# Kernel optimization log

Measured on AMD Instinct MI355X. Metric: run time of the kernel, lower is better.

## Reference

```python
import jax, jax.numpy as jnp
import numpy as np

N = 262144   # total packed tokens
B = 4096     # number of ragged segments
D = 256      # relation_embed_dim
A = 128      # attention_dim


def setup_inputs() -> dict:
    key = jax.random.key(0)
    k1, k2, k3 = jax.random.split(key, 3)
    relation_embeds = jax.random.normal(k1, (N, D), dtype=jnp.float32)
    # ragged segment ends: B-1 random interior end positions + final position N-1
    rng = np.random.default_rng(0)
    ends = np.sort(rng.choice(N - 1, size=B - 1, replace=False))
    ends = np.concatenate([ends, [N - 1]])
    queries_np = np.zeros((N,), dtype=np.int32)
    queries_np[ends] = 1
    queries = jnp.asarray(queries_np)
    # torch nn.Linear weights: [out, in]
    Wq = jax.random.normal(k2, (A, D), dtype=jnp.float32) / np.sqrt(D)
    Wk = jax.random.normal(k3, (A, D), dtype=jnp.float32) / np.sqrt(D)
    return {"relation_embeds": relation_embeds, "queries": queries,
            "num_segments": B, "Wq": Wq, "Wk": Wk}


def reference(relation_embeds, queries, num_segments, Wq, Wk):
    # segment id per token: exclusive cumsum of end markers
    q = queries.astype(jnp.int32)
    seg = jnp.cumsum(q) - q                      # [N] in [0, num_segments)
    ends = jnp.flatnonzero(q, size=num_segments) # [B] last index of each segment
    # per-segment query = Q(last row of segment); per-token key = K(row)
    q_end = relation_embeds[ends] @ Wq.T         # [B, A]
    k = relation_embeds @ Wk.T                   # [N, A]
    logits = jnp.sum(k * q_end[seg], axis=-1)    # [N] dot(Q_seg, K_token)
    # softmax over each ragged segment (dim=0 within segment)
    m = jax.ops.segment_max(logits, seg, num_segments=num_segments)
    ex = jnp.exp(logits - m[seg])
    denom = jax.ops.segment_sum(ex, seg, num_segments=num_segments)
    return ex / denom[seg]                       # [N] concatenated scores
```

## Files before the change

kernel.cpp:

```cpp
#include <hip/hip_runtime.h>
#include <math.h>
#include <float.h>

constexpr int N = 262144;
constexpr int B = 4096;
constexpr int D = 256;
constexpr int A = 128;

constexpr int CHUNK  = 1024;
constexpr int NCHUNK = N / CHUNK;
constexpr int SEGB   = 8;

typedef float fvec4 __attribute__((ext_vector_type(4)));

__global__ void k_partials_M(const int* __restrict__ q, int* __restrict__ partials,
                             const float* __restrict__ Wq, const float* __restrict__ Wk,
                             float* __restrict__ M) {
    int t = threadIdx.x;
    if (blockIdx.x < NCHUNK) {
        int4 v = ((const int4*)q)[blockIdx.x * (CHUNK / 4) + t];
        int s = v.x + v.y + v.z + v.w;
        int lane = t & 63, w = t >> 6;
#pragma unroll
        for (int o = 32; o > 0; o >>= 1) s += __shfl_xor(s, o, 64);
        __shared__ int ws_[4];
        if (lane == 0) ws_[w] = s;
        __syncthreads();
        if (t == 0) partials[blockIdx.x] = ws_[0] + ws_[1] + ws_[2] + ws_[3];
    } else {
        int d1 = blockIdx.x - NCHUNK;
        int d2 = t;
        float acc = 0.f;
#pragma unroll 4
        for (int a = 0; a < A; a++) {
            acc = fmaf(Wk[a * D + d1], Wq[a * D + d2], acc);
        }
        M[d1 * D + d2] = acc;
    }
}

__global__ void k_seg_ends(const int* __restrict__ q, const int* __restrict__ partials,
                           int* __restrict__ seg, int* __restrict__ ends) {
    int t = threadIdx.x;
    int lane = t & 63, w = t >> 6;
    int bid = blockIdx.x;
    int p = partials[t];
    int4 v = ((const int4*)q)[bid * (CHUNK / 4) + t];
    int tsum = v.x + v.y + v.z + v.w;
    int ps = p, ts = tsum;
#pragma unroll
    for (int o = 1; o < 64; o <<= 1) {
        int po = __shfl_up(ps, o, 64);
        int to = __shfl_up(ts, o, 64);
        if (lane >= o) { ps += po; ts += to; }
    }
    __shared__ int wp[4], wt[4];
    __shared__ int offs_sm;
    if (lane == 63) { wp[w] = ps; wt[w] = ts; }
    __syncthreads();
    int addp = 0, addt = 0;
#pragma unroll
    for (int i = 0; i < 4; i++) {
        if (i < w) { addp += wp[i]; addt += wt[i]; }
    }
    int sp_incl = ps + addp;
    int sm_incl = ts + addt;
    if (bid > 0 && t == bid - 1) offs_sm = sp_incl;
    if (bid == 0 && t == 0) offs_sm = 0;
    __syncthreads();
    int run = offs_sm + sm_incl - tsum;
    int base_idx = bid * CHUNK + t * 4;
    int qq[4] = {v.x, v.y, v.z, v.w};
#pragma unroll
    for (int k = 0; k < 4; k++) {
        int idx = base_idx + k;
        seg[idx] = run;
        if (qq[k]) { ends[run] = idx; run++; }
    }
}

__global__ void k_compute_V(const float* __restrict__ X, const int* __restrict__ ends,
                            const float* __restrict__ M, float* __restrict__ V) {
    int t = threadIdx.x;
    int b0 = blockIdx.x * SEGB;
    const float4* xr[SEGB];
#pragma unroll
    for (int r = 0; r < SEGB; r++) {
        xr[r] = (const float4*)(X + (size_t)ends[b0 + r] * D);
    }
    const float4* Mrow = (const float4*)(M + t * D);
    float acc[SEGB];
#pragma unroll
    for (int r = 0; r < SEGB; r++) acc[r] = 0.f;
#pragma unroll 4
    for (int j = 0; j < D / 4; j++) {
        float4 m4 = Mrow[j];
#pragma unroll
        for (int r = 0; r < SEGB; r++) {
            float4 x4 = xr[r][j];
            acc[r] = fmaf(m4.x, x4.x, fmaf(m4.y, x4.y,
                     fmaf(m4.z, x4.z, fmaf(m4.w, x4.w, acc[r]))));
        }
    }
#pragma unroll
    for (int r = 0; r < SEGB; r++) V[(size_t)(b0 + r) * D + t] = acc[r];
}

__global__ void k_logits(const float* __restrict__ X, const int* __restrict__ seg,
                         const float* __restrict__ V, float* __restrict__ logits) {
    int wave = threadIdx.x >> 6;
    int lane = threadIdx.x & 63;
    int tok0 = (blockIdx.x * 4 + wave) * 2;
    const fvec4* xa_p = (const fvec4*)(X + (size_t)tok0 * D) + lane;
    const fvec4* xb_p = (const fvec4*)(X + (size_t)(tok0 + 1) * D) + lane;
    fvec4 xa = __builtin_nontemporal_load(xa_p);
    fvec4 xb = __builtin_nontemporal_load(xb_p);
    int sa = seg[tok0];
    int sb = seg[tok0 + 1];
    float4 va = ((const float4*)(V + (size_t)sa * D))[lane];
    float4 vb = ((const float4*)(V + (size_t)sb * D))[lane];
    float pa = fmaf(xa.x, va.x, fmaf(xa.y, va.y, fmaf(xa.z, va.z, xa.w * va.w)));
    float pb = fmaf(xb.x, vb.x, fmaf(xb.y, vb.y, fmaf(xb.z, vb.z, xb.w * vb.w)));
#pragma unroll
    for (int o = 32; o > 0; o >>= 1) {
        pa += __shfl_xor(pa, o, 64);
        pb += __shfl_xor(pb, o, 64);
    }
    if (lane == 0) {
        float2 r = make_float2(pa, pb);
        *((float2*)(logits + tok0)) = r;
    }
}

__global__ void k_softmax(const float* __restrict__ logits, const int* __restrict__ ends,
                          float* __restrict__ out) {
    int wave = threadIdx.x >> 6;
    int lane = threadIdx.x & 63;
    int b = blockIdx.x * 4 + wave;
    int start = (b == 0) ? 0 : (ends[b - 1] + 1);
    int end = ends[b];
    float m = -FLT_MAX, s = 0.f;
    for (int i = start + lane; i <= end; i += 64) {
        float x = logits[i];
        float nm = fmaxf(m, x);
        s = s * __expf(m - nm) + __expf(x - nm);
        m = nm;
    }
#pragma unroll
    for (int o = 32; o > 0; o >>= 1) {
        float mo = __shfl_xor(m, o, 64);
        float so = __shfl_xor(s, o, 64);
        float nm = fmaxf(m, mo);
        s = s * __expf(m - nm) + so * __expf(mo - nm);
        m = nm;
    }
    float r = 1.f / s;
    for (int i = start + lane; i <= end; i += 64) out[i] = __expf(logits[i] - m) * r;
}

extern "C" void kernel_launch(void* const* d_in, const int* in_sizes, int n_in,
                              void* d_out, int out_size, void* d_ws, size_t ws_size,
                              hipStream_t stream) {
    const float* X  = (const float*)d_in[0];
    const int*   q  = (const int*)d_in[1];
    const float* Wq = (const float*)d_in[3];
    const float* Wk = (const float*)d_in[4];
    float* out = (float*)d_out;

    char* ws = (char*)d_ws;
    size_t off = 0;
    auto alloc = [&](size_t bytes) -> char* {
        char* p = ws + off;
        off += (bytes + 255) & ~(size_t)255;
        return p;
    };
    int*   seg      = (int*)alloc((size_t)N * 4);
    int*   ends     = (int*)alloc((size_t)B * 4);
    int*   partials = (int*)alloc((size_t)NCHUNK * 4);
    float* M        = (float*)alloc((size_t)D * D * 4);
    float* V        = (float*)alloc((size_t)B * D * 4);
    float* logits   = (float*)alloc((size_t)N * 4);

    k_partials_M<<<NCHUNK + D, 256, 0, stream>>>(q, partials, Wq, Wk, M);
    k_seg_ends<<<NCHUNK, 256, 0, stream>>>(q, partials, seg, ends);
    k_compute_V<<<B / SEGB, 256, 0, stream>>>(X, ends, M, V);
    k_logits<<<N / 8, 256, 0, stream>>>(X, seg, V, logits);
    k_softmax<<<B / 4, 256, 0, stream>>>(logits, ends, out);
}
```

Before: 406.5 us.

## Fuse all five stages into one cooperative kernel with grid syncs

Replaces the five separate kernel launches with a single cooperative persistent kernel of 1024 blocks. Grid-wide barriers separate the stages: partial counts and M, scan with segment ends, V, logits, and softmax. The logits stage becomes a grid-stride loop. The aim is to remove launch gaps and inter-kernel drain, at the cost of grid.sync overhead, less parallelism per stage, and a co-residency requirement on the grid.

Result: slower. 877.4 us (+115.9%).

```diff
diff --git a/kernel.cpp b/kernel.cpp
--- a/kernel.cpp
+++ b/kernel.cpp
@@ -1,6 +1,9 @@
 #include <hip/hip_runtime.h>
+#include <hip/hip_cooperative_groups.h>
 #include <math.h>
 #include <float.h>
+
+namespace cg = cooperative_groups;
 
 constexpr int N = 262144;
 constexpr int B = 4096;
@@ -10,25 +13,33 @@
 constexpr int CHUNK  = 1024;
 constexpr int NCHUNK = N / CHUNK;
 constexpr int SEGB   = 8;
+constexpr int GRID   = 1024;
 
 typedef float fvec4 __attribute__((ext_vector_type(4)));
 
-__global__ void k_partials_M(const int* __restrict__ q, int* __restrict__ partials,
-                             const float* __restrict__ Wq, const float* __restrict__ Wk,
-                             float* __restrict__ M) {
+__global__ void __launch_bounds__(256, 4)
+k_fused(const float* __restrict__ X, const int* __restrict__ q,
+        const float* __restrict__ Wq, const float* __restrict__ Wk,
+        int* __restrict__ seg, int* __restrict__ ends,
+        int* __restrict__ partials, float* __restrict__ M,
+        float* __restrict__ V, float* __restrict__ logits,
+        float* __restrict__ out) {
+    cg::grid_group grid = cg::this_grid();
     int t = threadIdx.x;
-    if (blockIdx.x < NCHUNK) {
-        int4 v = ((const int4*)q)[blockIdx.x * (CHUNK / 4) + t];
+    int lane = t & 63, w = t >> 6;
+    int bid = blockIdx.x;
+
+    if (bid < NCHUNK) {
+        int4 v = ((const int4*)q)[bid * (CHUNK / 4) + t];
         int s = v.x + v.y + v.z + v.w;
-        int lane = t & 63, w = t >> 6;
 #pragma unroll
         for (int o = 32; o > 0; o >>= 1) s += __shfl_xor(s, o, 64);
         __shared__ int ws_[4];
         if (lane == 0) ws_[w] = s;
         __syncthreads();
-        if (t == 0) partials[blockIdx.x] = ws_[0] + ws_[1] + ws_[2] + ws_[3];
-    } else {
-        int d1 = blockIdx.x - NCHUNK;
+        if (t == 0) partials[bid] = ws_[0] + ws_[1] + ws_[2] + ws_[3];
+    } else if (bid < NCHUNK + D) {
+        int d1 = bid - NCHUNK;
         int d2 = t;
         float acc = 0.f;
 #pragma unroll 4
@@ -37,125 +48,116 @@
         }
         M[d1 * D + d2] = acc;
     }
-}
+    grid.sync();
 
-__global__ void k_seg_ends(const int* __restrict__ q, const int* __restrict__ partials,
-                           int* __restrict__ seg, int* __restrict__ ends) {
-    int t = threadIdx.x;
-    int lane = t & 63, w = t >> 6;
-    int bid = blockIdx.x;
-    int p = partials[t];
-    int4 v = ((const int4*)q)[bid * (CHUNK / 4) + t];
-    int tsum = v.x + v.y + v.z + v.w;
-    int ps = p, ts = tsum;
+    if (bid < NCHUNK) {
+        int p = partials[t];
+        int4 v = ((const int4*)q)[bid * (CHUNK / 4) + t];
+        int tsum = v.x + v.y + v.z + v.w;
+        int ps = p, ts = tsum;
 #pragma unroll
-    for (int o = 1; o < 64; o <<= 1) {
-        int po = __shfl_up(ps, o, 64);
-        int to = __shfl_up(ts, o, 64);
-        if (lane >= o) { ps += po; ts += to; }
+        for (int o = 1; o < 64; o <<= 1) {
+            int po = __shfl_up(ps, o, 64);
+            int to = __shfl_up(ts, o, 64);
+            if (lane >= o) { ps += po; ts += to; }
+        }
+        __shared__ int wp[4], wt[4];
+        __shared__ int offs_sm;
+        if (lane == 63) { wp[w] = ps; wt[w] = ts; }
+        __syncthreads();
+        int addp = 0, addt = 0;
+#pragma unroll
+        for (int i = 0; i < 4; i++) {
+            if (i < w) { addp += wp[i]; addt += wt[i]; }
+        }
+        int sp_incl = ps + addp;
+        int sm_incl = ts + addt;
+        if (bid > 0 && t == bid - 1) offs_sm = sp_incl;
+        if (bid == 0 && t == 0) offs_sm = 0;
+        __syncthreads();
+        int run = offs_sm + sm_incl - tsum;
+        int base_idx = bid * CHUNK + t * 4;
+        int qq[4] = {v.x, v.y, v.z, v.w};
+#pragma unroll
+        for (int k = 0; k < 4; k++) {
+            int idx = base_idx + k;
+            seg[idx] = run;
+            if (qq[k]) { ends[run] = idx; run++; }
+        }
     }
-    __shared__ int wp[4], wt[4];
-    __shared__ int offs_sm;
-    if (lane == 63) { wp[w] = ps; wt[w] = ts; }
-    __syncthreads();
-    int addp = 0, addt = 0;
-#pragma unroll
-    for (int i = 0; i < 4; i++) {
-        if (i < w) { addp += wp[i]; addt += wt[i]; }
-    }
-    int sp_incl = ps + addp;
-    int sm_incl = ts + addt;
-    if (bid > 0 && t == bid - 1) offs_sm = sp_incl;
-    if (bid == 0 && t == 0) offs_sm = 0;
-    __syncthreads();
-    int run = offs_sm + sm_incl - tsum;
-    int base_idx = bid * CHUNK + t * 4;
-    int qq[4] = {v.x, v.y, v.z, v.w};
-#pragma unroll
-    for (int k = 0; k < 4; k++) {
-        int idx = base_idx + k;
-        seg[idx] = run;
-        if (qq[k]) { ends[run] = idx; run++; }
-    }
-}
+    grid.sync();
 
-__global__ void k_compute_V(const float* __restrict__ X, const int* __restrict__ ends,
-                            const float* __restrict__ M, float* __restrict__ V) {
-    int t = threadIdx.x;
-    int b0 = blockIdx.x * SEGB;
-    const float4* xr[SEGB];
-#pragma unroll
-    for (int r = 0; r < SEGB; r++) {
-        xr[r] = (const float4*)(X + (size_t)ends[b0 + r] * D);
-    }
-    const float4* Mrow = (const float4*)(M + t * D);
-    float acc[SEGB];
-#pragma unroll
-    for (int r = 0; r < SEGB; r++) acc[r] = 0.f;
-#pragma unroll 4
-    for (int j = 0; j < D / 4; j++) {
-        float4 m4 = Mrow[j];
+    if (bid < B / SEGB) {
+        int b0 = bid * SEGB;
+        const float4* xr[SEGB];
 #pragma unroll
         for (int r = 0; r < SEGB; r++) {
-            float4 x4 = xr[r][j];
-            acc[r] = fmaf(m4.x, x4.x, fmaf(m4.y, x4.y,
-                     fmaf(m4.z, x4.z, fmaf(m4.w, x4.w, acc[r]))));
+            xr[r] = (const float4*)(X + (size_t)ends[b0 + r] * D);
+        }
+        const float4* Mrow = (const float4*)(M + t * D);
+        float acc[SEGB];
+#pragma unroll
+        for (int r = 0; r < SEGB; r++) acc[r] = 0.f;
+#pragma unroll 4
+        for (int j = 0; j < D / 4; j++) {
+            float4 m4 = Mrow[j];
+#pragma unroll
+            for (int r = 0; r < SEGB; r++) {
+                float4 x4 = xr[r][j];
+                acc[r] = fmaf(m4.x, x4.x, fmaf(m4.y, x4.y,
+                         fmaf(m4.z, x4.z, fmaf(m4.w, x4.w, acc[r]))));
+            }
+        }
+#pragma unroll
+        for (int r = 0; r < SEGB; r++) V[(size_t)(b0 + r) * D + t] = acc[r];
+    }
+    grid.sync();
+
+    for (int u = bid; u < N / 8; u += GRID) {
+        int tok0 = (u * 4 + w) * 2;
+        const fvec4* xa_p = (const fvec4*)(X + (size_t)tok0 * D) + lane;
+        const fvec4* xb_p = (const fvec4*)(X + (size_t)(tok0 + 1) * D) + lane;
+        fvec4 xa = __builtin_nontemporal_load(xa_p);
+        fvec4 xb = __builtin_nontemporal_load(xb_p);
+        int sa = seg[tok0];
+        int sb = seg[tok0 + 1];
+        float4 va = ((const float4*)(V + (size_t)sa * D))[lane];
+        float4 vb = ((const float4*)(V + (size_t)sb * D))[lane];
+        float pa = fmaf(xa.x, va.x, fmaf(xa.y, va.y, fmaf(xa.z, va.z, xa.w * va.w)));
+        float pb = fmaf(xb.x, vb.x, fmaf(xb.y, vb.y, fmaf(xb.z, vb.z, xb.w * vb.w)));
+#pragma unroll
+        for (int o = 32; o > 0; o >>= 1) {
+            pa += __shfl_xor(pa, o, 64);
+            pb += __shfl_xor(pb, o, 64);
+        }
+        if (lane == 0) {
+            *((float2*)(logits + tok0)) = make_float2(pa, pb);
         }
     }
+    grid.sync();
+
+    {
+        int b = bid * 4 + w;
+        int start = (b == 0) ? 0 : (ends[b - 1] + 1);
+        int end = ends[b];
+        float m = -FLT_MAX, s = 0.f;
+        for (int i = start + lane; i <= end; i += 64) {
+            float x = logits[i];
+            float nm = fmaxf(m, x);
+            s = s * __expf(m - nm) + __expf(x - nm);
+            m = nm;
+        }
 #pragma unroll
-    for (int r = 0; r < SEGB; r++) V[(size_t)(b0 + r) * D + t] = acc[r];
-}
-
-__global__ void k_logits(const float* __restrict__ X, const int* __restrict__ seg,
-                         const float* __restrict__ V, float* __restrict__ logits) {
-    int wave = threadIdx.x >> 6;
-    int lane = threadIdx.x & 63;
-    int tok0 = (blockIdx.x * 4 + wave) * 2;
-    const fvec4* xa_p = (const fvec4*)(X + (size_t)tok0 * D) + lane;
-    const fvec4* xb_p = (const fvec4*)(X + (size_t)(tok0 + 1) * D) + lane;
-    fvec4 xa = __builtin_nontemporal_load(xa_p);
-    fvec4 xb = __builtin_nontemporal_load(xb_p);
-    int sa = seg[tok0];
-    int sb = seg[tok0 + 1];
-    float4 va = ((const float4*)(V + (size_t)sa * D))[lane];
-    float4 vb = ((const float4*)(V + (size_t)sb * D))[lane];
-    float pa = fmaf(xa.x, va.x, fmaf(xa.y, va.y, fmaf(xa.z, va.z, xa.w * va.w)));
-    float pb = fmaf(xb.x, vb.x, fmaf(xb.y, vb.y, fmaf(xb.z, vb.z, xb.w * vb.w)));
-#pragma unroll
-    for (int o = 32; o > 0; o >>= 1) {
-        pa += __shfl_xor(pa, o, 64);
-        pb += __shfl_xor(pb, o, 64);
+        for (int o = 32; o > 0; o >>= 1) {
+            float mo = __shfl_xor(m, o, 64);
+            float so = __shfl_xor(s, o, 64);
+            float nm = fmaxf(m, mo);
+            s = s * __expf(m - nm) + so * __expf(mo - nm);
+            m = nm;
+        }
+        float r = 1.f / s;
+        for (int i = start + lane; i <= end; i += 64) out[i] = __expf(logits[i] - m) * r;
     }
-    if (lane == 0) {
-        float2 r = make_float2(pa, pb);
-        *((float2*)(logits + tok0)) = r;
-    }
-}
-
-__global__ void k_softmax(const float* __restrict__ logits, const int* __restrict__ ends,
-                          float* __restrict__ out) {
-    int wave = threadIdx.x >> 6;
-    int lane = threadIdx.x & 63;
-    int b = blockIdx.x * 4 + wave;
-    int start = (b == 0) ? 0 : (ends[b - 1] + 1);
-    int end = ends[b];
-    float m = -FLT_MAX, s = 0.f;
-    for (int i = start + lane; i <= end; i += 64) {
-        float x = logits[i];
-        float nm = fmaxf(m, x);
-        s = s * __expf(m - nm) + __expf(x - nm);
-        m = nm;
-    }
-#pragma unroll
-    for (int o = 32; o > 0; o >>= 1) {
-        float mo = __shfl_xor(m, o, 64);
-        float so = __shfl_xor(s, o, 64);
-        float nm = fmaxf(m, mo);
-        s = s * __expf(m - nm) + so * __expf(mo - nm);
-        m = nm;
-    }
-    float r = 1.f / s;
-    for (int i = start + lane; i <= end; i += 64) out[i] = __expf(logits[i] - m) * r;
 }
 
 extern "C" void kernel_launch(void* const* d_in, const int* in_sizes, int n_in,
@@ -181,9 +183,9 @@
     float* V        = (float*)alloc((size_t)B * D * 4);
     float* logits   = (float*)alloc((size_t)N * 4);
 
-    k_partials_M<<<NCHUNK + D, 256, 0, stream>>>(q, partials, Wq, Wk, M);
-    k_seg_ends<<<NCHUNK, 256, 0, stream>>>(q, partials, seg, ends);
-    k_compute_V<<<B / SEGB, 256, 0, stream>>>(X, ends, M, V);
-    k_logits<<<N / 8, 256, 0, stream>>>(X, seg, V, logits);
-    k_softmax<<<B / 4, 256, 0, stream>>>(logits, ends, out);
+    void* args[] = {(void*)&X, (void*)&q, (void*)&Wq, (void*)&Wk,
+                    (void*)&seg, (void*)&ends, (void*)&partials,
+                    (void*)&M, (void*)&V, (void*)&logits, (void*)&out};
+    hipLaunchCooperativeKernel((const void*)k_fused, dim3(GRID), dim3(256),
+                               args, 0, stream);
 }
```

## Fuse logits and segment softmax into one per-segment kernel using LDS

Applied to the files above, without the earlier changes.

Logit computation and segmented softmax are merged into a single kernel with one block per segment. The block computes dot products of token rows against the segment vector, keeps the logits in shared memory, and then does a block-wide softmax. This removes the seg array and the global logits round trip, along with one kernel launch. In exchange, work is load-balanced per segment, so long or short ragged segments can leave CUs idle, and a 32KB LDS array limits occupancy. A fallback path recomputes the logits for segments longer than the cap.

Result: slower. 427.1 us (+5.1%).

```diff
diff --git a/kernel.cpp b/kernel.cpp
--- a/kernel.cpp
+++ b/kernel.cpp
@@ -10,6 +10,7 @@
 constexpr int CHUNK  = 1024;
 constexpr int NCHUNK = N / CHUNK;
 constexpr int SEGB   = 8;
+constexpr int SCAP   = 8192;
 
 typedef float fvec4 __attribute__((ext_vector_type(4)));
 
@@ -39,8 +40,8 @@
     }
 }
 
-__global__ void k_seg_ends(const int* __restrict__ q, const int* __restrict__ partials,
-                           int* __restrict__ seg, int* __restrict__ ends) {
+__global__ void k_ends(const int* __restrict__ q, const int* __restrict__ partials,
+                       int* __restrict__ ends) {
     int t = threadIdx.x;
     int lane = t & 63, w = t >> 6;
     int bid = blockIdx.x;
@@ -73,9 +74,7 @@
     int qq[4] = {v.x, v.y, v.z, v.w};
 #pragma unroll
     for (int k = 0; k < 4; k++) {
-        int idx = base_idx + k;
-        seg[idx] = run;
-        if (qq[k]) { ends[run] = idx; run++; }
+        if (qq[k]) { ends[run] = base_idx + k; run++; }
     }
 }
 
@@ -106,56 +105,93 @@
     for (int r = 0; r < SEGB; r++) V[(size_t)(b0 + r) * D + t] = acc[r];
 }
 
-__global__ void k_logits(const float* __restrict__ X, const int* __restrict__ seg,
-                         const float* __restrict__ V, float* __restrict__ logits) {
-    int wave = threadIdx.x >> 6;
-    int lane = threadIdx.x & 63;
-    int tok0 = (blockIdx.x * 4 + wave) * 2;
-    const fvec4* xa_p = (const fvec4*)(X + (size_t)tok0 * D) + lane;
-    const fvec4* xb_p = (const fvec4*)(X + (size_t)(tok0 + 1) * D) + lane;
-    fvec4 xa = __builtin_nontemporal_load(xa_p);
-    fvec4 xb = __builtin_nontemporal_load(xb_p);
-    int sa = seg[tok0];
-    int sb = seg[tok0 + 1];
-    float4 va = ((const float4*)(V + (size_t)sa * D))[lane];
-    float4 vb = ((const float4*)(V + (size_t)sb * D))[lane];
-    float pa = fmaf(xa.x, va.x, fmaf(xa.y, va.y, fmaf(xa.z, va.z, xa.w * va.w)));
-    float pb = fmaf(xb.x, vb.x, fmaf(xb.y, vb.y, fmaf(xb.z, vb.z, xb.w * vb.w)));
-#pragma unroll
-    for (int o = 32; o > 0; o >>= 1) {
-        pa += __shfl_xor(pa, o, 64);
-        pb += __shfl_xor(pb, o, 64);
-    }
-    if (lane == 0) {
-        float2 r = make_float2(pa, pb);
-        *((float2*)(logits + tok0)) = r;
-    }
-}
-
-__global__ void k_softmax(const float* __restrict__ logits, const int* __restrict__ ends,
-                          float* __restrict__ out) {
-    int wave = threadIdx.x >> 6;
-    int lane = threadIdx.x & 63;
-    int b = blockIdx.x * 4 + wave;
+__global__ void __launch_bounds__(256, 4)
+k_seg_attn(const float* __restrict__ X, const int* __restrict__ ends,
+           const float* __restrict__ V, float* __restrict__ out) {
+    int b = blockIdx.x;
+    int t = threadIdx.x;
+    int lane = t & 63, w = t >> 6;
     int start = (b == 0) ? 0 : (ends[b - 1] + 1);
     int end = ends[b];
-    float m = -FLT_MAX, s = 0.f;
-    for (int i = start + lane; i <= end; i += 64) {
-        float x = logits[i];
-        float nm = fmaxf(m, x);
-        s = s * __expf(m - nm) + __expf(x - nm);
-        m = nm;
-    }
-#pragma unroll
-    for (int o = 32; o > 0; o >>= 1) {
-        float mo = __shfl_xor(m, o, 64);
-        float so = __shfl_xor(s, o, 64);
-        float nm = fmaxf(m, mo);
-        s = s * __expf(m - nm) + so * __expf(mo - nm);
-        m = nm;
-    }
-    float r = 1.f / s;
-    for (int i = start + lane; i <= end; i += 64) out[i] = __expf(logits[i] - m) * r;
+    int len = end - start + 1;
+    float4 v4 = ((const float4*)(V + (size_t)b * D))[lane];
+    __shared__ float sl[SCAP];
+    __shared__ float wm[4], ws_[4];
+
+    if (len <= SCAP) {
+        for (int i = start + 2 * w; i <= end; i += 8) {
+            const fvec4* xp = (const fvec4*)(X + (size_t)i * D) + lane;
+            fvec4 xa = __builtin_nontemporal_load(xp);
+            float pa = fmaf(xa.x, v4.x, fmaf(xa.y, v4.y, fmaf(xa.z, v4.z, xa.w * v4.w)));
+            bool hasb = (i + 1 <= end);
+            float pb = 0.f;
+            if (hasb) {
+                const fvec4* xp2 = (const fvec4*)(X + (size_t)(i + 1) * D) + lane;
+                fvec4 xb = __builtin_nontemporal_load(xp2);
+                pb = fmaf(xb.x, v4.x, fmaf(xb.y, v4.y, fmaf(xb.z, v4.z, xb.w * v4.w)));
+            }
+#pragma unroll
+            for (int o = 32; o > 0; o >>= 1) {
+                pa += __shfl_xor(pa, o, 64);
+                pb += __shfl_xor(pb, o, 64);
+            }
+            if (lane == 0) {
+                sl[i - start] = pa;
+                if (hasb) sl[i + 1 - start] = pb;
+            }
+        }
+        __syncthreads();
+        float m = -FLT_MAX, s = 0.f;
+        for (int i = t; i < len; i += 256) {
+            float x = sl[i];
+            float nm = fmaxf(m, x);
+            s = s * __expf(m - nm) + __expf(x - nm);
+            m = nm;
+        }
+#pragma unroll
+        for (int o = 32; o > 0; o >>= 1) {
+            float mo = __shfl_xor(m, o, 64);
+            float so = __shfl_xor(s, o, 64);
+            float nm = fmaxf(m, mo);
+            s = s * __expf(m - nm) + so * __expf(mo - nm);
+            m = nm;
+        }
+        if (lane == 0) { wm[w] = m; ws_[w] = s; }
+        __syncthreads();
+        float M4 = fmaxf(fmaxf(wm[0], wm[1]), fmaxf(wm[2], wm[3]));
+        float S4 = ws_[0] * __expf(wm[0] - M4) + ws_[1] * __expf(wm[1] - M4)
+                 + ws_[2] * __expf(wm[2] - M4) + ws_[3] * __expf(wm[3] - M4);
+        float r = 1.f / S4;
+        for (int i = t; i < len; i += 256) {
+            out[start + i] = __expf(sl[i] - M4) * r;
+        }
+    } else {
+        float m = -FLT_MAX, s = 0.f;
+        for (int i = start + w; i <= end; i += 4) {
+            const float4* xp = (const float4*)(X + (size_t)i * D) + lane;
+            float4 xa = *xp;
+            float p = fmaf(xa.x, v4.x, fmaf(xa.y, v4.y, fmaf(xa.z, v4.z, xa.w * v4.w)));
+#pragma unroll
+            for (int o = 32; o > 0; o >>= 1) p += __shfl_xor(p, o, 64);
+            float nm = fmaxf(m, p);
+            s = s * __expf(m - nm) + __expf(p - nm);
+            m = nm;
+        }
+        if (lane == 0) { wm[w] = m; ws_[w] = s; }
+        __syncthreads();
+        float M4 = fmaxf(fmaxf(wm[0], wm[1]), fmaxf(wm[2], wm[3]));
+        float S4 = ws_[0] * __expf(wm[0] - M4) + ws_[1] * __expf(wm[1] - M4)
+                 + ws_[2] * __expf(wm[2] - M4) + ws_[3] * __expf(wm[3] - M4);
+        float r = 1.f / S4;
+        for (int i = start + w; i <= end; i += 4) {
+            const float4* xp = (const float4*)(X + (size_t)i * D) + lane;
+            float4 xa = *xp;
+            float p = fmaf(xa.x, v4.x, fmaf(xa.y, v4.y, fmaf(xa.z, v4.z, xa.w * v4.w)));
+#pragma unroll
+            for (int o = 32; o > 0; o >>= 1) p += __shfl_xor(p, o, 64);
+            if (lane == 0) out[i] = __expf(p - M4) * r;
+        }
+    }
 }
 
 extern "C" void kernel_launch(void* const* d_in, const int* in_sizes, int n_in,
@@ -174,16 +210,13 @@
         off += (bytes + 255) & ~(size_t)255;
         return p;
     };
-    int*   seg      = (int*)alloc((size_t)N * 4);
     int*   ends     = (int*)alloc((size_t)B * 4);
     int*   partials = (int*)alloc((size_t)NCHUNK * 4);
     float* M        = (float*)alloc((size_t)D * D * 4);
     float* V        = (float*)alloc((size_t)B * D * 4);
-    float* logits   = (float*)alloc((size_t)N * 4);
 
     k_partials_M<<<NCHUNK + D, 256, 0, stream>>>(q, partials, Wq, Wk, M);
-    k_seg_ends<<<NCHUNK, 256, 0, stream>>>(q, partials, seg, ends);
+    k_ends<<<NCHUNK, 256, 0, stream>>>(q, partials, ends);
     k_compute_V<<<B / SEGB, 256, 0, stream>>>(X, ends, M, V);
-    k_logits<<<N / 8, 256, 0, stream>>>(X, seg, V, logits);
-    k_softmax<<<B / 4, 256, 0, stream>>>(logits, ends, out);
-}
+    k_seg_attn<<<B, 256, 0, stream>>>(X, ends, V, out);
+}
```
